# Kernel optimization log

Measured on AMD Instinct MI355X. Metric: run time of the kernel, lower is better.

Reference implementation:

```python
import jax, jax.numpy as jnp
import numpy as np

N_QUBITS = 12
N_LAYERS = 4
BATCH = 4096
OUT_DIM = 12


def _ry(theta):
    theta = jnp.asarray(theta, jnp.float32)
    c, s = jnp.cos(theta / 2), jnp.sin(theta / 2)
    U = jnp.stack([jnp.stack([c, -s], -1), jnp.stack([s, c], -1)], -2)
    return U.astype(jnp.complex64)


def _rx(theta):
    theta = jnp.asarray(theta, jnp.float32)
    c = jnp.cos(theta / 2).astype(jnp.complex64)
    s = (-1j) * jnp.sin(theta / 2).astype(jnp.complex64)
    return jnp.stack([jnp.stack([c, s], -1), jnp.stack([s, c], -1)], -2)


def _rz(theta):
    theta = jnp.asarray(theta, jnp.float32)
    e = jnp.exp((-0.5j) * theta.astype(jnp.complex64))
    z = jnp.zeros_like(e)
    return jnp.stack([jnp.stack([e, z], -1), jnp.stack([z, jnp.conj(e)], -1)], -2)


def _apply_1q(psi, U, w):
    # psi: (B,) + (2,)*n; U: (2,2) shared gate or (B,2,2) per-sample gate
    psi = jnp.moveaxis(psi, w + 1, 1)
    if U.ndim == 2:
        psi = jnp.einsum('ij,bj...->bi...', U, psi)
    else:
        psi = jnp.einsum('bij,bj...->bi...', U, psi)
    return jnp.moveaxis(psi, 1, w + 1)


def _cnot(psi, c, t):
    # flip target axis where control bit == 1
    psi = jnp.moveaxis(psi, (c + 1, t + 1), (1, 2))
    psi = psi.at[:, 1].set(psi[:, 1, ::-1])
    return jnp.moveaxis(psi, (1, 2), (c + 1, t + 1))


def _pauli_z_signs(n):
    idx = np.arange(2 ** n)
    bits = (idx[None, :] >> (n - 1 - np.arange(n))[:, None]) & 1  # wire 0 = MSB
    return jnp.asarray(1.0 - 2.0 * bits, jnp.float32)  # (n, 2^n)


def _quantum_forward(x, quantum_weights):
    b, n = x.shape[0], N_QUBITS
    # tf.nn.l2_normalize(sample, axis=0) per sample
    xn = x * jax.lax.rsqrt(jnp.maximum(jnp.sum(x * x, axis=1, keepdims=True), 1e-12))
    # angle encoding: pi * x / (max|x| + 1e-8)
    angles = jnp.pi * xn / (jnp.max(jnp.abs(xn), axis=1, keepdims=True) + 1e-8)
    psi = jnp.zeros((b, 2 ** n), jnp.complex64).at[:, 0].set(1.0)
    psi = psi.reshape((b,) + (2,) * n)
    # data encoding: RY(angles[i]) on wire i (per-sample batched gates)
    for i in range(n):
        psi = _apply_1q(psi, _ry(angles[:, i]), i)
    # variational layers: RX/RY/RZ per qubit, then CNOT ring
    for layer in range(N_LAYERS):
        base = layer * 3 * n
        for i in range(n):
            p = base + 3 * i
            psi = _apply_1q(psi, _rx(quantum_weights[p]), i)
            psi = _apply_1q(psi, _ry(quantum_weights[p + 1]), i)
            psi = _apply_1q(psi, _rz(quantum_weights[p + 2]), i)
        for i in range(n):
            psi = _cnot(psi, i, (i + 1) % n)
    psi = psi.reshape(b, -1)
    probs = jnp.real(psi) ** 2 + jnp.imag(psi) ** 2  # (B, 2^n)
    return probs @ _pauli_z_signs(n).T  # (B, n): <Z_i> per qubit


def setup_inputs() -> dict:
    key = jax.random.key(0)
    k1, k2, k3 = jax.random.split(key, 3)
    n_params = 3 * N_QUBITS * N_LAYERS
    return {
        'x': jax.random.normal(k1, (BATCH, N_QUBITS), jnp.float32),
        'quantum_weights': jax.random.uniform(k2, (n_params,), jnp.float32, -0.05, 0.05),
        'dense_w': jax.random.normal(k3, (N_QUBITS, OUT_DIM), jnp.float32) / np.sqrt(N_QUBITS),
        'dense_b': jnp.zeros((OUT_DIM,), jnp.float32),
    }


def reference(x, quantum_weights, dense_w, dense_b):
    q = _quantum_forward(x, quantum_weights)
    return jnp.tanh(q @ dense_w + dense_b)
```

## Files before the change

### kernel.cpp

```cpp
#include <hip/hip_runtime.h>
#include <math.h>

#define NQ   12
#define NL   4
#define GBLK 256
#define QBLK 512
#define SOFF(i) ((i) * 8192)

typedef float v4f  __attribute__((ext_vector_type(4)));
typedef __fp16 v8h __attribute__((ext_vector_type(8)));
typedef unsigned v4u __attribute__((ext_vector_type(4)));

__device__ __forceinline__ constexpr int sigma_inv_c(int i) {
    int j = i;
    for (int c = 0; c < NQ; ++c) {
        int t = (c + 1) % NQ;
        int cb = (j >> (NQ - 1 - c)) & 1;
        j ^= cb << (NQ - 1 - t);
    }
    return j;
}

__device__ __forceinline__ constexpr int lswz(int l) {
    return l ^ (((l >> 3) ^ (l >> 7)) & 7);
}

__device__ __forceinline__ unsigned pk2(float a, float b) {
    return __builtin_bit_cast(unsigned, __builtin_amdgcn_cvt_pkrtz(a, b));
}

__device__ __forceinline__ int fslot(int k, int n) {
    return ((k >> 3) * 16 + n) * 8 + (k & 7);
}

__global__ __launch_bounds__(GBLK) void gate_kernel(
    const float* __restrict__ qw, __fp16* __restrict__ gout)
{
    __shared__ float G[NQ][8];
    const int t = threadIdx.x;
    const int mat = blockIdx.x;
    const int layer = mat / 3, ph = mat - 3 * layer;
    if (t < NQ) {
        const int p = layer * 3 * NQ + 3 * t;
        float t1 = qw[p], t2 = qw[p + 1], t3 = qw[p + 2];
        float a, b, c, d, gr, h;
        sincosf(0.5f * t1, &b, &a);
        sincosf(0.5f * t2, &d, &c);
        sincosf(0.5f * t3, &h, &gr);
        float m00r =  c * a, m00i =  d * b;
        float m01r = -d * a, m01i = -c * b;
        float m10r =  d * a, m10i = -c * b;
        float m11r =  c * a, m11i = -d * b;
        float* g = G[t];
        g[0] = gr * m00r + h * m00i;  g[1] = gr * m00i - h * m00r;
        g[2] = gr * m01r + h * m01i;  g[3] = gr * m01i - h * m01r;
        g[4] = gr * m10r - h * m10i;  g[5] = gr * m10i + h * m10r;
        g[6] = gr * m11r - h * m11i;  g[7] = gr * m11i + h * m11r;
    }
    __syncthreads();
    const int n = t & 15, r = t >> 4;
    const int wbase = (ph == 0) ? 8 : (ph == 1) ? 4 : 0;
    float cr = 1.f, ci = 0.f;
    #pragma unroll
    for (int b = 0; b < 4; ++b) {
        const float* g = G[wbase + b];
        const int rb = (r >> (3 - b)) & 1, nb = (n >> (3 - b)) & 1;
        const float er = g[(nb * 2 + rb) * 2], ei = g[(nb * 2 + rb) * 2 + 1];
        const float xr = cr * er - ci * ei, xi = cr * ei + ci * er;
        cr = xr; ci = xi;
    }
    __fp16* b1 = gout + (mat * 2 + 0) * 512;
    __fp16* b2 = gout + (mat * 2 + 1) * 512;
    b1[fslot(2 * r, n)]     = (__fp16)cr;
    b1[fslot(2 * r + 1, n)] = (__fp16)(-ci);
    b2[fslot(2 * r, n)]     = (__fp16)ci;
    b2[fslot(2 * r + 1, n)] = (__fp16)cr;
}

#define READ_FRAGS(AF, SRC)                                                 \
    _Pragma("unroll")                                                       \
    for (int j = 0; j < 2; ++j)                                             \
        AF[j] = __builtin_bit_cast(v8h, *(const uint4*)&sh[(SRC) +          \
                    lswz((((wv) << 6) | ((2 * qh + j) << 4) | nn) * 4 + g) * 8]);

#define BLOAD(MAT)                                                          \
    const v8h b1 = gf[((MAT) * 2 + 0) * 64 + lane];                         \
    const v8h b2 = gf[((MAT) * 2 + 1) * 64 + lane];

#define BLOAD2(MATB, MATC)                                                  \
    const v8h b1 = gf[((MATB) * 2 + 0) * 64 + lane];                        \
    const v8h b2 = gf[((MATB) * 2 + 1) * 64 + lane];                        \
    const v8h c1 = gf[((MATC) * 2 + 0) * 64 + lane];                        \
    const v8h c2 = gf[((MATC) * 2 + 1) * 64 + lane];

#define MFMA_ONE(AF)                                                        \
    _Pragma("unroll")                                                       \
    for (int j = 0; j < 2; ++j) {                                           \
        d1[j] = __builtin_amdgcn_mfma_f32_16x16x32_f16(AF[j], b1, zf, 0, 0, 0); \
        d2[j] = __builtin_amdgcn_mfma_f32_16x16x32_f16(AF[j], b2, zf, 0, 0, 0); \
    }

#define PACK_AF(AF)                                                         \
    _Pragma("unroll")                                                       \
    for (int j = 0; j < 2; ++j) {                                           \
        v4u t;                                                              \
        _Pragma("unroll")                                                   \
        for (int rg = 0; rg < 4; ++rg) t[rg] = pk2(d1[j][rg], d2[j][rg]);   \
        AF[j] = __builtin_bit_cast(v8h, t);                                 \
    }

#define MFMA_CC(AF)                                                         \
    _Pragma("unroll")                                                       \
    for (int j = 0; j < 2; ++j) {                                           \
        d1[j] = __builtin_amdgcn_mfma_f32_16x16x32_f16(AF[j], c1, zf, 0, 0, 0); \
        d2[j] = __builtin_amdgcn_mfma_f32_16x16x32_f16(AF[j], c2, zf, 0, 0, 0); \
    }

#define SCHB __builtin_amdgcn_sched_barrier(0);

#define WRITE_COLS(DST)                                                     \
    _Pragma("unroll")                                                       \
    for (int j = 0; j < 2; ++j) {                                           \
        const int CCn = (nn << 4) | (wv << 2) | (2 * qh + j);               \
        *(uint4*)&sh[(DST) + lswz(CCn * 4 + g) * 8] =                       \
            make_uint4(pk2(d1[j].x, d2[j].x), pk2(d1[j].y, d2[j].y),        \
                       pk2(d1[j].z, d2[j].z), pk2(d1[j].w, d2[j].w));       \
    }

#define WRITE_SIGMA2(DST)                                                   \
    _Pragma("unroll")                                                       \
    for (int j = 0; j < 2; ++j) {                                           \
        const int ij = ifix2 ^ (j ? sigma_inv_c(1) : 0);                    \
        _Pragma("unroll")                                                   \
        for (int rg = 0; rg < 4; ++rg) {                                    \
            const int ii = ij ^ sigma_inv_c(rg << 4);                       \
            *(unsigned*)&sh[(DST) + lswz(ii >> 2) * 8 + (ii & 3) * 2] =     \
                pk2(d1[j][rg], d2[j][rg]);                                  \
        }                                                                   \
    }

#define WHT_EPI2(OFF)                                                       \
    { float p8[8];                                                          \
      _Pragma("unroll")                                                     \
      for (int j = 0; j < 2; ++j)                                           \
          _Pragma("unroll")                                                 \
          for (int rg = 0; rg < 4; ++rg)                                    \
              p8[j * 4 + rg] = d1[j][rg] * d1[j][rg] + d2[j][rg] * d2[j][rg]; \
      _Pragma("unroll")                                                     \
      for (int st = 1; st < 8; st <<= 1) {                                  \
          _Pragma("unroll")                                                 \
          for (int i = 0; i < 8; ++i) {                                     \
              if (!(i & st)) {                                              \
                  const float a = p8[i], b = p8[i ^ st];                    \
                  p8[i] = a + b; p8[i ^ st] = a - b;                        \
              }                                                             \
          }                                                                 \
      }                                                                     \
      float vals[NQ];                                                       \
      _Pragma("unroll")                                                     \
      for (int w = 0; w < NQ; ++w) {                                        \
          const int sb = 11 - w;                                            \
          const int fj  = (sigma_inv_c(0x001) >> sb) & 1;                   \
          const int frh = (sigma_inv_c(0x020) >> sb) & 1;                   \
          const int frl = (sigma_inv_c(0x010) >> sb) & 1;                   \
          const float v = p8[fj * 4 + frh * 2 + frl];                       \
          vals[w] = ((ifix2 >> sb) & 1) ? -v : v;                           \
      }                                                                     \
      _Pragma("unroll")                                                     \
      for (int m = 1; m <= 8; m <<= 1) {                                    \
          _Pragma("unroll")                                                 \
          for (int w = 0; w < NQ; ++w) vals[w] += __shfl_xor(vals[w], m);   \
      }                                                                     \
      if ((lane & 15) == 0) {                                               \
          _Pragma("unroll")                                                 \
          for (int w = 0; w < NQ; ++w)                                      \
              red[(OFF) + W * 48 + (lane >> 4) * 12 + w] = vals[w];         \
      } }

__global__ __launch_bounds__(QBLK) void qsim_kernel(
    const float* __restrict__ x,
    const __fp16* __restrict__ gates,
    const float* __restrict__ dw,
    const float* __restrict__ db,
    float* __restrict__ out,
    int batch)
{
    __shared__ __align__(16) __fp16 sh[32768];
    float* xv    = (float*)sh;
    float* enc_c = (float*)sh + 64;
    float* enc_s = (float*)sh + 128;
    float* red   = (float*)sh;

    const int tid  = threadIdx.x;
    const int lane = tid & 63;
    const int W    = tid >> 6;
    const int wv   = W & 3;
    const int qh   = W >> 2;
    const int base = 4 * blockIdx.x;
    int ss[4];
    #pragma unroll
    for (int i = 0; i < 4; ++i) {
        int s = base + i;
        ss[i] = (s < batch) ? s : batch - 1;
    }
    const int nn = lane & 15, g = lane >> 4;
    const v8h* gf = (const v8h*)gates;
    const v4f zf = {0.f, 0.f, 0.f, 0.f};

    if (tid < 4 * NQ) {
        const int smp = tid / NQ, j = tid - smp * NQ;
        xv[tid] = x[ss[smp] * NQ + j];
    }
    __syncthreads();
    if (tid < 4 * NQ) {
        const int b0 = (tid / NQ) * NQ;
        float sum = 0.f;
        #pragma unroll
        for (int j = 0; j < NQ; ++j) sum += xv[b0 + j] * xv[b0 + j];
        float inv = rsqrtf(fmaxf(sum, 1e-12f));
        float mx = 0.f;
        #pragma unroll
        for (int j = 0; j < NQ; ++j) mx = fmaxf(mx, fabsf(xv[b0 + j] * inv));
        float ang = 3.14159265358979323846f * (xv[tid] * inv) / (mx + 1e-8f);
        float cc, sn;
        sincosf(0.5f * ang, &sn, &cc);
        enc_c[tid] = cc; enc_s[tid] = sn;
    }
    __syncthreads();

    v8h af0[2], af1[2], af2[2], af3[2];
    #define PICK(SMP, WW, B) ((B) ? enc_s[(SMP) * NQ + (WW)] : enc_c[(SMP) * NQ + (WW)])
    #define INIT_AF(AF, SMP)                                                \
    {   float R4[4];                                                        \
        _Pragma("unroll")                                                   \
        for (int t = 0; t < 4; ++t) {                                       \
            const int r = 4 * g + t;                                        \
            R4[t] = PICK(SMP, 8, (r >> 3) & 1) * PICK(SMP, 9, (r >> 2) & 1) \
                  * PICK(SMP, 10, (r >> 1) & 1) * PICK(SMP, 11, r & 1);     \
        }                                                                   \
        const float Pfix = PICK(SMP, 0, (wv >> 1) & 1) * PICK(SMP, 1, wv & 1) \
                         * PICK(SMP, 4, (nn >> 3) & 1) * PICK(SMP, 5, (nn >> 2) & 1) \
                         * PICK(SMP, 6, (nn >> 1) & 1) * PICK(SMP, 7, nn & 1); \
        _Pragma("unroll")                                                   \
        for (int j = 0; j < 2; ++j) {                                       \
            const float Pq = Pfix * PICK(SMP, 2, qh) * PICK(SMP, 3, j);     \
            _Pragma("unroll")                                               \
            for (int t = 0; t < 4; ++t) {                                   \
                AF[j][2 * t]     = (__fp16)(Pq * R4[t]);                    \
                AF[j][2 * t + 1] = (__fp16)0.f;                             \
            }                                                               \
        }                                                                   \
    }
    INIT_AF(af0, 0)
    INIT_AF(af1, 1)
    INIT_AF(af2, 2)
    INIT_AF(af3, 3)
    #undef PICK
    __syncthreads();

    const int ifix2 = sigma_inv_c((nn << 8) | (g << 6) | (wv << 2) | (qh << 1));

    v4f d1[2], d2[2];
    #define READ4                                                           \
        READ_FRAGS(af0, SOFF(0)) READ_FRAGS(af1, SOFF(1))                   \
        READ_FRAGS(af2, SOFF(2)) READ_FRAGS(af3, SOFF(3))
    #define COLS4(MAT)                                                      \
        { BLOAD(MAT)                                                        \
          MFMA_ONE(af0) WRITE_COLS(SOFF(0)) SCHB                            \
          MFMA_ONE(af1) WRITE_COLS(SOFF(1)) SCHB                            \
          MFMA_ONE(af2) WRITE_COLS(SOFF(2)) SCHB                            \
          MFMA_ONE(af3) WRITE_COLS(SOFF(3)) }
    #define CHAIN_S(AF, DST)                                                \
        MFMA_ONE(AF) PACK_AF(AF) MFMA_CC(AF) WRITE_SIGMA2(DST)
    #define CHAIN_E(AF, EOFF)                                               \
        MFMA_ONE(AF) PACK_AF(AF) MFMA_CC(AF) WHT_EPI2(EOFF)

    #pragma unroll 1
    for (int l = 0; l < NL; ++l) {
        if (l > 0) {
            READ4
            __syncthreads();
        }
        COLS4(l * 3 + 0)
        __syncthreads();

        READ4
        __syncthreads();
        if (l < NL - 1) {
            { BLOAD2(l * 3 + 1, l * 3 + 2)
              CHAIN_S(af0, SOFF(0)) SCHB
              CHAIN_S(af1, SOFF(1)) SCHB
              CHAIN_S(af2, SOFF(2)) SCHB
              CHAIN_S(af3, SOFF(3)) }
            __syncthreads();
        } else {
            { BLOAD2(l * 3 + 1, l * 3 + 2)
              CHAIN_E(af0, 0)    SCHB
              CHAIN_E(af1, 384)  SCHB
              CHAIN_E(af2, 768)  SCHB
              CHAIN_E(af3, 1152) }
        }
    }

    __syncthreads();
    if (tid < 4 * NQ) {
        const int smp = tid / NQ, w = tid - smp * NQ;
        float acc = 0.f;
        #pragma unroll
        for (int k = 0; k < 32; ++k) acc += red[smp * 384 + k * 12 + w];
        red[1536 + tid] = acc;
    }
    __syncthreads();
    if (tid < 4 * NQ) {
        const int smp = tid / NQ, o = tid - smp * NQ;
        const float* rv = red + 1536 + smp * NQ;
        float v = db[o];
        #pragma unroll
        for (int w = 0; w < NQ; ++w) v += rv[w] * dw[w * NQ + o];
        out[ss[smp] * NQ + o] = tanhf(v);
    }
}

extern "C" void kernel_launch(void* const* d_in, const int* in_sizes, int n_in,
                              void* d_out, int out_size, void* d_ws, size_t ws_size,
                              hipStream_t stream) {
    const float* x  = (const float*)d_in[0];
    const float* qw = (const float*)d_in[1];
    const float* dw = (const float*)d_in[2];
    const float* db = (const float*)d_in[3];
    float* out = (float*)d_out;
    __fp16* gates = (__fp16*)d_ws;
    int batch = in_sizes[0] / NQ;
    int nblk = (batch + 3) / 4;
    gate_kernel<<<12, GBLK, 0, stream>>>(qw, gates);
    qsim_kernel<<<nblk, QBLK, 0, stream>>>(x, gates, dw, db, out, batch);
}
```

Before: 107.9 us.

## Fuse gate matrix construction into simulation kernel and derive second B fragment

Removes the separate gate_kernel launch and instead has each qsim block compute the 12 fused 16x16 gate matrices from the weights into shared memory. The B operands are then read from LDS rather than global memory. Only the first fragment is stored; the second is derived by swapping and negating fp16 halves in registers. This removes a kernel launch and the dependent global round-trip. In exchange every block repeats the gate computation, shared memory grows to 80 KB, and that may lower occupancy.

After: 108.2 us. About the same (+0.3%).

```diff
diff --git a/kernel.cpp b/kernel.cpp
--- a/kernel.cpp
+++ b/kernel.cpp
@@ -3,9 +3,8 @@
 
 #define NQ   12
 #define NL   4
-#define GBLK 256
 #define QBLK 512
-#define SOFF(i) ((i) * 8192)
+#define SOFF(i) (8192 + (i) * 8192)
 
 typedef float v4f  __attribute__((ext_vector_type(4)));
 typedef __fp16 v8h __attribute__((ext_vector_type(8)));
@@ -33,48 +32,15 @@
     return ((k >> 3) * 16 + n) * 8 + (k & 7);
 }
 
-__global__ __launch_bounds__(GBLK) void gate_kernel(
-    const float* __restrict__ qw, __fp16* __restrict__ gout)
-{
-    __shared__ float G[NQ][8];
-    const int t = threadIdx.x;
-    const int mat = blockIdx.x;
-    const int layer = mat / 3, ph = mat - 3 * layer;
-    if (t < NQ) {
-        const int p = layer * 3 * NQ + 3 * t;
-        float t1 = qw[p], t2 = qw[p + 1], t3 = qw[p + 2];
-        float a, b, c, d, gr, h;
-        sincosf(0.5f * t1, &b, &a);
-        sincosf(0.5f * t2, &d, &c);
-        sincosf(0.5f * t3, &h, &gr);
-        float m00r =  c * a, m00i =  d * b;
-        float m01r = -d * a, m01i = -c * b;
-        float m10r =  d * a, m10i = -c * b;
-        float m11r =  c * a, m11i = -d * b;
-        float* g = G[t];
-        g[0] = gr * m00r + h * m00i;  g[1] = gr * m00i - h * m00r;
-        g[2] = gr * m01r + h * m01i;  g[3] = gr * m01i - h * m01r;
-        g[4] = gr * m10r - h * m10i;  g[5] = gr * m10i + h * m10r;
-        g[6] = gr * m11r - h * m11i;  g[7] = gr * m11i + h * m11r;
-    }
-    __syncthreads();
-    const int n = t & 15, r = t >> 4;
-    const int wbase = (ph == 0) ? 8 : (ph == 1) ? 4 : 0;
-    float cr = 1.f, ci = 0.f;
+__device__ __forceinline__ v8h derive_b2(v8h b) {
+    v4u w = __builtin_bit_cast(v4u, b);
+    v4u r;
     #pragma unroll
-    for (int b = 0; b < 4; ++b) {
-        const float* g = G[wbase + b];
-        const int rb = (r >> (3 - b)) & 1, nb = (n >> (3 - b)) & 1;
-        const float er = g[(nb * 2 + rb) * 2], ei = g[(nb * 2 + rb) * 2 + 1];
-        const float xr = cr * er - ci * ei, xi = cr * ei + ci * er;
-        cr = xr; ci = xi;
-    }
-    __fp16* b1 = gout + (mat * 2 + 0) * 512;
-    __fp16* b2 = gout + (mat * 2 + 1) * 512;
-    b1[fslot(2 * r, n)]     = (__fp16)cr;
-    b1[fslot(2 * r + 1, n)] = (__fp16)(-ci);
-    b2[fslot(2 * r, n)]     = (__fp16)ci;
-    b2[fslot(2 * r + 1, n)] = (__fp16)cr;
+    for (int i = 0; i < 4; ++i) {
+        const unsigned rot = (w[i] >> 16) | (w[i] << 16);
+        r[i] = rot ^ 0x8000u;
+    }
+    return __builtin_bit_cast(v8h, r);
 }
 
 #define READ_FRAGS(AF, SRC)                                                 \
@@ -84,14 +50,14 @@
                     lswz((((wv) << 6) | ((2 * qh + j) << 4) | nn) * 4 + g) * 8]);
 
 #define BLOAD(MAT)                                                          \
-    const v8h b1 = gf[((MAT) * 2 + 0) * 64 + lane];                         \
-    const v8h b2 = gf[((MAT) * 2 + 1) * 64 + lane];
+    const v8h b1 = *(const v8h*)&sh[(MAT) * 512 + lane * 8];                \
+    const v8h b2 = derive_b2(b1);
 
 #define BLOAD2(MATB, MATC)                                                  \
-    const v8h b1 = gf[((MATB) * 2 + 0) * 64 + lane];                        \
-    const v8h b2 = gf[((MATB) * 2 + 1) * 64 + lane];                        \
-    const v8h c1 = gf[((MATC) * 2 + 0) * 64 + lane];                        \
-    const v8h c2 = gf[((MATC) * 2 + 1) * 64 + lane];
+    const v8h b1 = *(const v8h*)&sh[(MATB) * 512 + lane * 8];               \
+    const v8h b2 = derive_b2(b1);                                           \
+    const v8h c1 = *(const v8h*)&sh[(MATC) * 512 + lane * 8];               \
+    const v8h c2 = derive_b2(c1);
 
 #define MFMA_ONE(AF)                                                        \
     _Pragma("unroll")                                                       \
@@ -179,17 +145,19 @@
 
 __global__ __launch_bounds__(QBLK) void qsim_kernel(
     const float* __restrict__ x,
-    const __fp16* __restrict__ gates,
+    const float* __restrict__ qw,
     const float* __restrict__ dw,
     const float* __restrict__ db,
     float* __restrict__ out,
     int batch)
 {
-    __shared__ __align__(16) __fp16 sh[32768];
-    float* xv    = (float*)sh;
-    float* enc_c = (float*)sh + 64;
-    float* enc_s = (float*)sh + 128;
-    float* red   = (float*)sh;
+    __shared__ __align__(16) __fp16 sh[40960];
+    float* fb    = (float*)(sh + 6144);
+    float* xv    = fb;
+    float* enc_c = fb + 64;
+    float* enc_s = fb + 128;
+    float* Gt    = fb + 192;
+    float* red   = (float*)(sh + SOFF(0));
 
     const int tid  = threadIdx.x;
     const int lane = tid & 63;
@@ -204,7 +172,6 @@
         ss[i] = (s < batch) ? s : batch - 1;
     }
     const int nn = lane & 15, g = lane >> 4;
-    const v8h* gf = (const v8h*)gates;
     const v4f zf = {0.f, 0.f, 0.f, 0.f};
 
     if (tid < 4 * NQ) {
@@ -225,8 +192,45 @@
         float cc, sn;
         sincosf(0.5f * ang, &sn, &cc);
         enc_c[tid] = cc; enc_s[tid] = sn;
-    }
-    __syncthreads();
+    } else if (tid >= 64 && tid < 64 + NL * NQ) {
+        const int t = tid - 64;
+        const int p = (t / NQ) * 3 * NQ + 3 * (t % NQ);
+        float t1 = qw[p], t2 = qw[p + 1], t3 = qw[p + 2];
+        float a, b, c, d, gr, h;
+        sincosf(0.5f * t1, &b, &a);
+        sincosf(0.5f * t2, &d, &c);
+        sincosf(0.5f * t3, &h, &gr);
+        float m00r =  c * a, m00i =  d * b;
+        float m01r = -d * a, m01i = -c * b;
+        float m10r =  d * a, m10i = -c * b;
+        float m11r =  c * a, m11i = -d * b;
+        float* gg = Gt + t * 8;
+        gg[0] = gr * m00r + h * m00i;  gg[1] = gr * m00i - h * m00r;
+        gg[2] = gr * m01r + h * m01i;  gg[3] = gr * m01i - h * m01r;
+        gg[4] = gr * m10r - h * m10i;  gg[5] = gr * m10i + h * m10r;
+        gg[6] = gr * m11r - h * m11i;  gg[7] = gr * m11i + h * m11r;
+    }
+    __syncthreads();
+
+    #pragma unroll
+    for (int e = 0; e < 6; ++e) {
+        const int idx = tid * 6 + e;
+        const int mat = idx >> 8, rn = idx & 255;
+        const int r = rn >> 4, n = rn & 15;
+        const int layer = mat / 3, ph = mat - 3 * layer;
+        const int wbase = (ph == 0) ? 8 : (ph == 1) ? 4 : 0;
+        float cr = 1.f, ci = 0.f;
+        #pragma unroll
+        for (int b = 0; b < 4; ++b) {
+            const float* gg = Gt + (layer * NQ + wbase + b) * 8;
+            const int rb = (r >> (3 - b)) & 1, nb = (n >> (3 - b)) & 1;
+            const float er = gg[(nb * 2 + rb) * 2], ei = gg[(nb * 2 + rb) * 2 + 1];
+            const float xr = cr * er - ci * ei, xi = cr * ei + ci * er;
+            cr = xr; ci = xi;
+        }
+        sh[mat * 512 + fslot(2 * r, n)]     = (__fp16)cr;
+        sh[mat * 512 + fslot(2 * r + 1, n)] = (__fp16)(-ci);
+    }
 
     v8h af0[2], af1[2], af2[2], af3[2];
     #define PICK(SMP, WW, B) ((B) ? enc_s[(SMP) * NQ + (WW)] : enc_c[(SMP) * NQ + (WW)])
@@ -329,9 +333,7 @@
     const float* dw = (const float*)d_in[2];
     const float* db = (const float*)d_in[3];
     float* out = (float*)d_out;
-    __fp16* gates = (__fp16*)d_ws;
     int batch = in_sizes[0] / NQ;
     int nblk = (batch + 3) / 4;
-    gate_kernel<<<12, GBLK, 0, stream>>>(qw, gates);
-    qsim_kernel<<<nblk, QBLK, 0, stream>>>(x, gates, dw, db, out, batch);
-}
+    qsim_kernel<<<nblk, QBLK, 0, stream>>>(x, qw, dw, db, out, batch);
+}
```
